# Optimization experiments

Measured on AMD Instinct MI355X. Metric: run time of the kernel, lower is better.

Reference implementation:

```python
import jax, jax.numpy as jnp
import numpy as np

CONF_THRES = 0.25
IOU_THRES = 0.45
MAX_DET = 1000
MAX_WH = 4096.0   # class offset for per-class NMS (yolov5 trick)
TOPK = 2048       # pre-NMS candidate cap (fixed-shape stand-in for max_nms)


def _xywh2xyxy(b):
    cx, cy, w, h = b[..., 0], b[..., 1], b[..., 2], b[..., 3]
    return jnp.stack([cx - w * 0.5, cy - h * 0.5, cx + w * 0.5, cy + h * 0.5], axis=-1)


def _box_iou(a, b):
    # a, b: [K, 4] in xyxy -> [K, K] pairwise IoU
    lt = jnp.maximum(a[:, None, :2], b[None, :, :2])
    rb = jnp.minimum(a[:, None, 2:], b[None, :, 2:])
    wh = jnp.clip(rb - lt, 0.0)
    inter = wh[..., 0] * wh[..., 1]
    area_a = (a[:, 2] - a[:, 0]) * (a[:, 3] - a[:, 1])
    area_b = (b[:, 2] - b[:, 0]) * (b[:, 3] - b[:, 1])
    return inter / (area_a[:, None] + area_b[None, :] - inter + 1e-7)


def _nms_single(pred):
    # pred: [N, 5+C] = (cx, cy, w, h, obj, cls...)
    obj = pred[:, 4]
    cls_prob = pred[:, 5:]
    cls_conf = jnp.max(cls_prob, axis=-1)
    cls_id = jnp.argmax(cls_prob, axis=-1)
    score = obj * cls_conf                      # conf = obj_conf * cls_conf (best class)
    valid = (obj > CONF_THRES) & (score > CONF_THRES)
    score = jnp.where(valid, score, 0.0)
    boxes = _xywh2xyxy(pred[:, :4])

    # keep top-K candidates by confidence (sorted descending)
    tops, idx = jax.lax.top_k(score, TOPK)
    boxes_k = boxes[idx]                        # [K, 4]
    cls_k = cls_id[idx]                         # [K]
    val_k = tops > 0.0

    # per-class NMS via class offset
    shifted = boxes_k + (cls_k.astype(boxes_k.dtype) * MAX_WH)[:, None]
    iou = _box_iou(shifted, shifted)            # [K, K]

    j = jnp.arange(TOPK)

    def body(i, keep):
        # if box i survives, suppress lower-scored boxes with IoU > thresh
        sup = keep[i] & (iou[i] > IOU_THRES) & (j > i)
        return keep & ~sup

    keep = jax.lax.fori_loop(0, TOPK, body, val_k)

    # gather up to MAX_DET kept detections (already score-sorted)
    fs, fi = jax.lax.top_k(jnp.where(keep, tops, -1.0), MAX_DET)
    ok = fs > 0.0
    det_boxes = jnp.where(ok[:, None], boxes_k[fi], 0.0)
    det_score = jnp.where(ok, tops[fi], 0.0)
    det_cls = jnp.where(ok, cls_k[fi].astype(det_boxes.dtype), -1.0)
    # [MAX_DET, 6] = (x1, y1, x2, y2, conf, cls); padded rows have conf 0, cls -1
    return jnp.concatenate([det_boxes, det_score[:, None], det_cls[:, None]], axis=-1)


def setup_inputs() -> dict:
    key = jax.random.key(0)
    raw = jax.random.uniform(key, (16, 25200, 85), dtype=jnp.float32)
    xy = raw[..., 0:2] * 640.0            # centers within a 640x640 image
    wh = raw[..., 2:4] * 120.0 + 2.0      # box sizes in [2, 122]
    rest = raw[..., 4:]                   # obj + class probs in [0, 1)
    pred = jnp.concatenate([xy, wh, rest], axis=-1)
    return {"pred": pred}


def reference(pred):
    return jax.vmap(_nms_single)(pred)
```

## Files before the change

kernel.cpp:

```cpp
#include <hip/hip_runtime.h>
#include <stdint.h>

#pragma clang fp contract(off)

#define BB 16
#define NN 25200
#define ROW 85
#define NCLS 80
#define TK 2048
#define SORTN 4096
#define NBIN 4096
#define MAXDET 1000
#define CONF 0.25f
#define IOUT 0.45f
#define MAXWH 4096.0f
#define SROWS 64

typedef float fvec4 __attribute__((ext_vector_type(4)));

#define AS1 __attribute__((address_space(1)))
#define AS3 __attribute__((address_space(3)))

__global__ __launch_bounds__(128) void score_kernel(const float* __restrict__ pred,
                                                    float* __restrict__ scores,
                                                    uint8_t* __restrict__ cls,
                                                    unsigned int* __restrict__ hist) {
  __shared__ __align__(16) float srow[SROWS * ROW];
  const int tile = blockIdx.x;
  const int b = blockIdx.y;
  const int tid = threadIdx.x;
  const int lane = tid & 63;
  const int row0 = tile * SROWS;
  int nrows = NN - row0;
  if (nrows > SROWS) nrows = SROWS;
  const char* gsrc = (const char*)(pred + ((size_t)b * NN + row0) * ROW);
  const int nbytes = nrows * ROW * 4;
  for (int off = tid * 16; off < nbytes; off += 128 * 16) {
    __builtin_amdgcn_global_load_lds((AS1 void*)(gsrc + off),
                                     (AS3 void*)((char*)srow + (off - lane * 16)),
                                     16, 0, 0);
  }
  __builtin_amdgcn_s_waitcnt(0);
  __syncthreads();
  if (tid < nrows) {
    const int n = row0 + tid;
    const float* r = srow + tid * ROW;
    float obj = r[4];
    float best = r[5];
    int bid = 0;
#pragma unroll
    for (int c = 1; c < NCLS; ++c) {
      float p = r[5 + c];
      if (p > best) { best = p; bid = c; }
    }
    float score = obj * best;
    bool valid = (obj > CONF) && (score > CONF);
    float sout = valid ? score : 0.0f;
    scores[(size_t)b * NN + n] = sout;
    cls[(size_t)b * NN + n] = (uint8_t)bid;
    if (valid) {
      unsigned int u = __float_as_uint(sout);
      unsigned int bin = (u - 0x3E800001u) >> 12;
      if (bin > NBIN - 1) bin = NBIN - 1;
      atomicAdd(&hist[(size_t)b * NBIN + bin], 1u);
    }
  }
}

__global__ __launch_bounds__(1024) void mega_kernel(const float* __restrict__ pred,
                                                    const float* __restrict__ scores,
                                                    const uint8_t* __restrict__ cls,
                                                    const unsigned int* __restrict__ hist,
                                                    float* __restrict__ out) {
  const int b = blockIdx.x;
  const int t = threadIdx.x;
  const int w = t >> 6;
  const int lane = t & 63;
  __shared__ unsigned long long skey[SORTN];
  __shared__ unsigned int sh[NBIN];
  __shared__ unsigned int soff[NBIN];
  __shared__ float sx1[TK], sy1[TK], sx2[TK], sy2[TK];
  __shared__ float stop[TK];
  __shared__ unsigned short scls[TK];
  __shared__ unsigned short cgrpL[TK];
  __shared__ unsigned char skp[TK];
  __shared__ int spart[1024];
  __shared__ int ccnt[NCLS];
  __shared__ int coffs[NCLS + 1];
  __shared__ int sP;

  if (t == 0) sP = 0;
  for (int i = t; i < NBIN; i += 1024) sh[i] = hist[(size_t)b * NBIN + i];
  for (int i = t; i < SORTN; i += 1024) skey[i] = 0ull;
  __syncthreads();

  int loc[4];
  int ssum = 0;
#pragma unroll
  for (int k = 0; k < 4; ++k) {
    loc[k] = (int)sh[NBIN - 1 - (4 * t + k)];
    ssum += loc[k];
  }
  spart[t] = ssum;
  __syncthreads();
  for (int o = 1; o < 1024; o <<= 1) {
    int v = (t >= o) ? spart[t - o] : 0;
    __syncthreads();
    spart[t] += v;
    __syncthreads();
  }
  int run = spart[t] - ssum;
#pragma unroll
  for (int k = 0; k < 4; ++k) {
    int bin = NBIN - 1 - (4 * t + k);
    soff[bin] = (unsigned int)run;
    if (run < TK && run + loc[k] >= TK) sP = bin;
    run += loc[k];
  }
  __syncthreads();
  const int P = sP;
  for (int i = t; i < NBIN; i += 1024) sh[i] = 0u;
  __syncthreads();

  const float* sc = scores + (size_t)b * NN;
  for (int n = t; n < NN; n += 1024) {
    unsigned int u = __float_as_uint(sc[n]);
    if (u > 0x3E800000u) {
      unsigned int bin = (u - 0x3E800001u) >> 12;
      if (bin > NBIN - 1) bin = NBIN - 1;
      if ((int)bin >= P) {
        unsigned int pos = soff[bin] + atomicAdd(&sh[bin], 1u);
        if (pos < SORTN)
          skey[pos] = ((unsigned long long)u << 32) | (unsigned int)(~n);
      }
    }
  }
  __syncthreads();

  for (int bin = P + w; bin < NBIN; bin += 16) {
    int s = (int)sh[bin];
    if (s < 2) continue;
    int base = (int)soff[bin];
    if (base >= SORTN) continue;
    if (base + s > SORTN) s = SORTN - base;
    if (s < 2) continue;
    if (s <= 64) {
      bool act = lane < s;
      unsigned long long key = act ? skey[base + lane] : 0ull;
      int rank = 0;
      for (int j = 0; j < s; ++j) {
        unsigned long long kj = skey[base + j];
        rank += (act && kj > key) ? 1 : 0;
      }
      if (act) skey[base + rank] = key;
    } else {
      for (int pass = 0; pass < s; ++pass) {
        for (int p = base + (pass & 1) + 2 * lane; p + 1 < base + s; p += 128) {
          unsigned long long a = skey[p], b2 = skey[p + 1];
          if (a < b2) { skey[p] = b2; skey[p + 1] = a; }
        }
        asm volatile("" ::: "memory");
      }
    }
    asm volatile("" ::: "memory");
  }
  __syncthreads();

  for (int i = t; i < TK; i += 1024) {
    unsigned long long key = skey[i];
    unsigned int ub = (unsigned int)(key >> 32);
    if (ub == 0u) {
      stop[i] = 0.0f;
      scls[i] = (unsigned short)0xFFFFu;
      skp[i] = 0;
      sx1[i] = 0.f; sy1[i] = 0.f; sx2[i] = 0.f; sy2[i] = 0.f;
    } else {
      int idx = (int)(~(unsigned int)key);
      stop[i] = __uint_as_float(ub);
      scls[i] = (unsigned short)cls[(size_t)b * NN + idx];
      skp[i] = 1;
      const float* rowp = pred + ((size_t)b * NN + idx) * ROW;
      float cx = rowp[0], cy = rowp[1], w2 = rowp[2], h2 = rowp[3];
      float hw = w2 * 0.5f, hh = h2 * 0.5f;
      sx1[i] = cx - hw; sy1[i] = cy - hh; sx2[i] = cx + hw; sy2[i] = cy + hh;
    }
  }
  __syncthreads();

#pragma unroll
  for (int k = 0; k < 5; ++k) {
    int c = w + 16 * k;
    int cnt = 0;
    for (int base2 = 0; base2 < TK; base2 += 64) {
      bool match = ((int)scls[base2 + lane] == c);
      cnt += (int)__popcll(__ballot(match));
    }
    if (lane == 0) ccnt[c] = cnt;
  }
  __syncthreads();
  if (t == 0) {
    int r2 = 0;
    for (int c = 0; c < NCLS; ++c) { coffs[c] = r2; r2 += ccnt[c]; }
    coffs[NCLS] = r2;
  }
  __syncthreads();
#pragma unroll
  for (int k = 0; k < 5; ++k) {
    int c = w + 16 * k;
    int run2 = coffs[c];
    for (int base2 = 0; base2 < TK; base2 += 64) {
      bool match = ((int)scls[base2 + lane] == c);
      unsigned long long bal = __ballot(match);
      int r3 = (int)__popcll(bal & ((1ull << lane) - 1ull));
      if (match) cgrpL[run2 + r3] = (unsigned short)(base2 + lane);
      run2 += (int)__popcll(bal);
    }
  }
  __syncthreads();

  for (int k = 0; k < 5; ++k) {
    int c = w + 16 * k;
    int start = coffs[c];
    int m = coffs[c + 1] - start;
    if (m <= 0) continue;
    int nq = (m + 63) >> 6;
    unsigned int km = 0;
    for (int q = 0; q < nq; ++q)
      if (lane + (q << 6) < m) km |= (1u << q);
    float b0x1 = 0.f, b0y1 = 0.f, b0x2 = 0.f, b0y2 = 0.f;
    if (lane < m) {
      int e0 = cgrpL[start + lane];
      b0x1 = sx1[e0]; b0y1 = sy1[e0]; b0x2 = sx2[e0]; b0y2 = sy2[e0];
    }
    for (int i = 0; i < m; ++i) {
      int q = i >> 6;
      unsigned int kmi = __shfl(km, i & 63);
      if (!((kmi >> q) & 1u)) continue;
      float ax1, ay1, ax2, ay2;
      if (q == 0) {
        ax1 = __shfl(b0x1, i); ay1 = __shfl(b0y1, i);
        ax2 = __shfl(b0x2, i); ay2 = __shfl(b0y2, i);
      } else {
        int ei = cgrpL[start + i];
        ax1 = sx1[ei]; ay1 = sy1[ei]; ax2 = sx2[ei]; ay2 = sy2[ei];
      }
      float aarea = (ax2 - ax1) * (ay2 - ay1);
      if ((km & 1u) && lane > i) {
        float ltx = fmaxf(ax1, b0x1), lty = fmaxf(ay1, b0y1);
        float rbx = fminf(ax2, b0x2), rby = fminf(ay2, b0y2);
        float iw = fmaxf(rbx - ltx, 0.0f);
        float ih = fmaxf(rby - lty, 0.0f);
        float inter = iw * ih;
        float barea = (b0x2 - b0x1) * (b0y2 - b0y1);
        float iou = inter / (aarea + barea - inter + 1e-7f);
        if (iou > IOUT) km &= ~1u;
      }
      for (int q2 = 1; q2 < nq; ++q2) {
        int j = lane + (q2 << 6);
        if (((km >> q2) & 1u) && j > i && j < m) {
          int ej = cgrpL[start + j];
          float jx1 = sx1[ej], jy1 = sy1[ej], jx2 = sx2[ej], jy2 = sy2[ej];
          float ltx = fmaxf(ax1, jx1), lty = fmaxf(ay1, jy1);
          float rbx = fminf(ax2, jx2), rby = fminf(ay2, jy2);
          float iw = fmaxf(rbx - ltx, 0.0f);
          float ih = fmaxf(rby - lty, 0.0f);
          float inter = iw * ih;
          float barea = (jx2 - jx1) * (jy2 - jy1);
          float iou = inter / (aarea + barea - inter + 1e-7f);
          if (iou > IOUT) km &= ~(1u << q2);
        }
      }
    }
    for (int q = 0; q < nq; ++q) {
      int j = lane + (q << 6);
      if (j < m) skp[cgrpL[start + j]] = (unsigned char)((km >> q) & 1u);
    }
  }
  __syncthreads();

  int kp0 = (int)skp[2 * t];
  int kp1 = (int)skp[2 * t + 1];
  int cnt2 = kp0 + kp1;
  spart[t] = cnt2;
  __syncthreads();
  for (int o = 1; o < 1024; o <<= 1) {
    int v = (t >= o) ? spart[t - o] : 0;
    __syncthreads();
    spart[t] += v;
    __syncthreads();
  }
  int r4 = spart[t] - cnt2;
  int K = spart[1023];
#pragma unroll
  for (int k = 0; k < 2; ++k) {
    int kp = (k == 0) ? kp0 : kp1;
    if (kp) {
      if (r4 < MAXDET) {
        int j = 2 * t + k;
        float* o = out + ((size_t)b * MAXDET + r4) * 6;
        o[0] = sx1[j]; o[1] = sy1[j]; o[2] = sx2[j]; o[3] = sy2[j];
        o[4] = stop[j];
        o[5] = (float)scls[j];
      }
      ++r4;
    }
  }
  int Kc = K < MAXDET ? K : MAXDET;
  for (int r2 = Kc + t; r2 < MAXDET; r2 += 1024) {
    float* o = out + ((size_t)b * MAXDET + r2) * 6;
    o[0] = 0.0f; o[1] = 0.0f; o[2] = 0.0f; o[3] = 0.0f; o[4] = 0.0f; o[5] = -1.0f;
  }
}

extern "C" void kernel_launch(void* const* d_in, const int* in_sizes, int n_in,
                              void* d_out, int out_size, void* d_ws, size_t ws_size,
                              hipStream_t stream) {
  const float* pred = (const float*)d_in[0];
  float* out = (float*)d_out;

  char* ws = (char*)d_ws;
  size_t off = 0;
  float*        scores = (float*)(ws + off);        off += (size_t)BB * NN * 4;
  uint8_t*      cls    = (uint8_t*)(ws + off);      off += (size_t)BB * NN;
  off = (off + 255) & ~(size_t)255;
  unsigned int* hist   = (unsigned int*)(ws + off); off += (size_t)BB * NBIN * 4;
  (void)ws_size; (void)in_sizes; (void)n_in; (void)out_size;

  hipMemsetAsync(hist, 0, (size_t)BB * NBIN * 4, stream);
  score_kernel<<<dim3((NN + SROWS - 1) / SROWS, BB), 128, 0, stream>>>(pred, scores, cls, hist);
  mega_kernel<<<BB, 1024, 0, stream>>>(pred, scores, cls, hist, out);
}
```

Measured before the change: 290.4 us.

## Split per-image mega kernel into scan, scatter, sort-emit and NMS kernels

The monolithic per-image kernel, which ran on only 16 workgroups, is split into separate kernels. A small scan kernel builds bin offsets with wave shuffles, a grid-wide scatter spreads the candidate keys across many blocks, and a multi-block sort/emit kernel ranks bins and gathers boxes into global buffers. A final kernel then runs NMS from those buffers, using a shuffle-based scan for compaction. The goal is to raise parallelism for the select/sort phase, which was serialized in 16 blocks. The cost is extra launches and round-trips through global memory, plus global-memory bubble sorts for large bins.

```diff
diff --git a/kernel.cpp b/kernel.cpp
--- a/kernel.cpp
+++ b/kernel.cpp
@@ -13,7 +13,6 @@
 #define MAXDET 1000
 #define CONF 0.25f
 #define IOUT 0.45f
-#define MAXWH 4096.0f
 #define SROWS 64
 
 typedef float fvec4 __attribute__((ext_vector_type(4)));
@@ -67,122 +66,166 @@
   }
 }
 
-__global__ __launch_bounds__(1024) void mega_kernel(const float* __restrict__ pred,
-                                                    const float* __restrict__ scores,
-                                                    const uint8_t* __restrict__ cls,
-                                                    const unsigned int* __restrict__ hist,
-                                                    float* __restrict__ out) {
+__global__ __launch_bounds__(256) void scan_kernel(const unsigned int* __restrict__ hist,
+                                                   unsigned int* __restrict__ gsoff,
+                                                   int* __restrict__ gP,
+                                                   int* __restrict__ gtot) {
+  const int b = blockIdx.x;
+  const int t = threadIdx.x;
+  const int w = t >> 6, lane = t & 63;
+  const unsigned int* h = hist + (size_t)b * NBIN;
+  unsigned int loc[16];
+  int ssum = 0;
+#pragma unroll
+  for (int k = 0; k < 16; ++k) {
+    loc[k] = h[NBIN - 1 - (16 * t + k)];
+    ssum += (int)loc[k];
+  }
+  int v = ssum;
+  for (int o = 1; o < 64; o <<= 1) { int u = __shfl_up(v, o); if (lane >= o) v += u; }
+  __shared__ int sw[4];
+  __shared__ int sfound;
+  if (t == 0) sfound = 0;
+  if (lane == 63) sw[w] = v;
+  __syncthreads();
+  int wbase = 0;
+  for (int i = 0; i < w; ++i) wbase += sw[i];
+  const int total = sw[0] + sw[1] + sw[2] + sw[3];
+  int run = wbase + v - ssum;
+#pragma unroll
+  for (int k = 0; k < 16; ++k) {
+    int bin = NBIN - 1 - (16 * t + k);
+    gsoff[(size_t)b * NBIN + bin] = (unsigned int)run;
+    int c = (int)loc[k];
+    if (run < TK && run + c >= TK) {
+      gP[b] = bin;
+      gtot[b] = run + c;
+      sfound = 1;
+    }
+    run += c;
+  }
+  __syncthreads();
+  if (t == 0 && !sfound) { gP[b] = 0; gtot[b] = total; }
+}
+
+__global__ __launch_bounds__(1024) void scatter_kernel(const float* __restrict__ scores,
+                                                       const unsigned int* __restrict__ gsoff,
+                                                       const int* __restrict__ gP,
+                                                       unsigned int* __restrict__ gcnt,
+                                                       unsigned long long* __restrict__ gskey) {
+  const int b = blockIdx.y;
+  const int n = blockIdx.x * 1024 + threadIdx.x;
+  if (n >= NN) return;
+  const unsigned int P = (unsigned int)gP[b];
+  unsigned int u = __float_as_uint(scores[(size_t)b * NN + n]);
+  if (u > 0x3E800000u) {
+    unsigned int bin = (u - 0x3E800001u) >> 12;
+    if (bin > NBIN - 1) bin = NBIN - 1;
+    if (bin >= P) {
+      unsigned int pos = gsoff[(size_t)b * NBIN + bin] +
+                         atomicAdd(&gcnt[(size_t)b * NBIN + bin], 1u);
+      if (pos < SORTN)
+        gskey[(size_t)b * SORTN + pos] = ((unsigned long long)u << 32) | (unsigned int)(~n);
+    }
+  }
+}
+
+__device__ __forceinline__ void emit_one(const float* __restrict__ pred,
+                                         const uint8_t* __restrict__ cls,
+                                         int b, int pos, unsigned long long key,
+                                         float* __restrict__ gtops,
+                                         fvec4* __restrict__ gbox,
+                                         int* __restrict__ gcls) {
+  int idx = (int)(~(unsigned int)key);
+  gtops[(size_t)b * TK + pos] = __uint_as_float((unsigned int)(key >> 32));
+  gcls[(size_t)b * TK + pos] = (int)cls[(size_t)b * NN + idx];
+  const float* rowp = pred + ((size_t)b * NN + idx) * ROW;
+  float cx = rowp[0], cy = rowp[1], w2 = rowp[2], h2 = rowp[3];
+  float hw = w2 * 0.5f, hh = h2 * 0.5f;
+  fvec4 bb4;
+  bb4[0] = cx - hw; bb4[1] = cy - hh; bb4[2] = cx + hw; bb4[3] = cy + hh;
+  gbox[(size_t)b * TK + pos] = bb4;
+}
+
+__global__ __launch_bounds__(256) void sortemit_kernel(const float* __restrict__ pred,
+                                                       const uint8_t* __restrict__ cls,
+                                                       const unsigned int* __restrict__ gsoff,
+                                                       const unsigned int* __restrict__ gcnt,
+                                                       const int* __restrict__ gP,
+                                                       unsigned long long* __restrict__ gskey,
+                                                       float* __restrict__ gtops,
+                                                       fvec4* __restrict__ gbox,
+                                                       int* __restrict__ gcls) {
+  const int b = blockIdx.y;
+  const int g = blockIdx.x;
+  const int w = threadIdx.x >> 6;
+  const int lane = threadIdx.x & 63;
+  const int P = gP[b];
+  for (int bin = P + g * 4 + w; bin < NBIN; bin += 32) {
+    int s = (int)gcnt[(size_t)b * NBIN + bin];
+    if (s <= 0) continue;
+    int base = (int)gsoff[(size_t)b * NBIN + bin];
+    if (base >= TK) continue;
+    if (base + s > SORTN) s = SORTN - base;
+    if (s <= 64) {
+      unsigned long long key = (lane < s) ? gskey[(size_t)b * SORTN + base + lane] : 0ull;
+      int rank = 0;
+      for (int jj = 0; jj < s; ++jj) {
+        unsigned long long kj = __shfl(key, jj);
+        rank += (kj > key) ? 1 : 0;
+      }
+      int pos = base + rank;
+      if (lane < s && pos < TK)
+        emit_one(pred, cls, b, pos, key, gtops, gbox, gcls);
+    } else {
+      unsigned long long* seg = gskey + (size_t)b * SORTN + base;
+      for (int pass = 0; pass < s; ++pass) {
+        for (int p = (pass & 1) + 2 * lane; p + 1 < s; p += 128) {
+          unsigned long long a = seg[p], c2 = seg[p + 1];
+          if (a < c2) { seg[p] = c2; seg[p + 1] = a; }
+        }
+        __threadfence();
+      }
+      for (int i = lane; i < s; i += 64) {
+        int pos = base + i;
+        if (pos < TK) emit_one(pred, cls, b, pos, seg[i], gtops, gbox, gcls);
+      }
+    }
+  }
+}
+
+__global__ __launch_bounds__(1024) void final_kernel(const float* __restrict__ gtops,
+                                                     const fvec4* __restrict__ gbox,
+                                                     const int* __restrict__ gcls,
+                                                     const int* __restrict__ gtot,
+                                                     float* __restrict__ out) {
   const int b = blockIdx.x;
   const int t = threadIdx.x;
   const int w = t >> 6;
   const int lane = t & 63;
-  __shared__ unsigned long long skey[SORTN];
-  __shared__ unsigned int sh[NBIN];
-  __shared__ unsigned int soff[NBIN];
   __shared__ float sx1[TK], sy1[TK], sx2[TK], sy2[TK];
   __shared__ float stop[TK];
   __shared__ unsigned short scls[TK];
   __shared__ unsigned short cgrpL[TK];
   __shared__ unsigned char skp[TK];
-  __shared__ int spart[1024];
   __shared__ int ccnt[NCLS];
   __shared__ int coffs[NCLS + 1];
-  __shared__ int sP;
-
-  if (t == 0) sP = 0;
-  for (int i = t; i < NBIN; i += 1024) sh[i] = hist[(size_t)b * NBIN + i];
-  for (int i = t; i < SORTN; i += 1024) skey[i] = 0ull;
-  __syncthreads();
-
-  int loc[4];
-  int ssum = 0;
-#pragma unroll
-  for (int k = 0; k < 4; ++k) {
-    loc[k] = (int)sh[NBIN - 1 - (4 * t + k)];
-    ssum += loc[k];
-  }
-  spart[t] = ssum;
-  __syncthreads();
-  for (int o = 1; o < 1024; o <<= 1) {
-    int v = (t >= o) ? spart[t - o] : 0;
-    __syncthreads();
-    spart[t] += v;
-    __syncthreads();
-  }
-  int run = spart[t] - ssum;
-#pragma unroll
-  for (int k = 0; k < 4; ++k) {
-    int bin = NBIN - 1 - (4 * t + k);
-    soff[bin] = (unsigned int)run;
-    if (run < TK && run + loc[k] >= TK) sP = bin;
-    run += loc[k];
-  }
-  __syncthreads();
-  const int P = sP;
-  for (int i = t; i < NBIN; i += 1024) sh[i] = 0u;
-  __syncthreads();
-
-  const float* sc = scores + (size_t)b * NN;
-  for (int n = t; n < NN; n += 1024) {
-    unsigned int u = __float_as_uint(sc[n]);
-    if (u > 0x3E800000u) {
-      unsigned int bin = (u - 0x3E800001u) >> 12;
-      if (bin > NBIN - 1) bin = NBIN - 1;
-      if ((int)bin >= P) {
-        unsigned int pos = soff[bin] + atomicAdd(&sh[bin], 1u);
-        if (pos < SORTN)
-          skey[pos] = ((unsigned long long)u << 32) | (unsigned int)(~n);
-      }
-    }
-  }
-  __syncthreads();
-
-  for (int bin = P + w; bin < NBIN; bin += 16) {
-    int s = (int)sh[bin];
-    if (s < 2) continue;
-    int base = (int)soff[bin];
-    if (base >= SORTN) continue;
-    if (base + s > SORTN) s = SORTN - base;
-    if (s < 2) continue;
-    if (s <= 64) {
-      bool act = lane < s;
-      unsigned long long key = act ? skey[base + lane] : 0ull;
-      int rank = 0;
-      for (int j = 0; j < s; ++j) {
-        unsigned long long kj = skey[base + j];
-        rank += (act && kj > key) ? 1 : 0;
-      }
-      if (act) skey[base + rank] = key;
+  __shared__ int swsum[16];
+
+  int npos = gtot[b];
+  if (npos > TK) npos = TK;
+  for (int i = t; i < TK; i += 1024) {
+    if (i < npos) {
+      fvec4 bb4 = gbox[(size_t)b * TK + i];
+      sx1[i] = bb4[0]; sy1[i] = bb4[1]; sx2[i] = bb4[2]; sy2[i] = bb4[3];
+      stop[i] = gtops[(size_t)b * TK + i];
+      scls[i] = (unsigned short)gcls[(size_t)b * TK + i];
+      skp[i] = 1;
     } else {
-      for (int pass = 0; pass < s; ++pass) {
-        for (int p = base + (pass & 1) + 2 * lane; p + 1 < base + s; p += 128) {
-          unsigned long long a = skey[p], b2 = skey[p + 1];
-          if (a < b2) { skey[p] = b2; skey[p + 1] = a; }
-        }
-        asm volatile("" ::: "memory");
-      }
-    }
-    asm volatile("" ::: "memory");
-  }
-  __syncthreads();
-
-  for (int i = t; i < TK; i += 1024) {
-    unsigned long long key = skey[i];
-    unsigned int ub = (unsigned int)(key >> 32);
-    if (ub == 0u) {
-      stop[i] = 0.0f;
+      sx1[i] = 0.f; sy1[i] = 0.f; sx2[i] = 0.f; sy2[i] = 0.f;
+      stop[i] = 0.f;
       scls[i] = (unsigned short)0xFFFFu;
       skp[i] = 0;
-      sx1[i] = 0.f; sy1[i] = 0.f; sx2[i] = 0.f; sy2[i] = 0.f;
-    } else {
-      int idx = (int)(~(unsigned int)key);
-      stop[i] = __uint_as_float(ub);
-      scls[i] = (unsigned short)cls[(size_t)b * NN + idx];
-      skp[i] = 1;
-      const float* rowp = pred + ((size_t)b * NN + idx) * ROW;
-      float cx = rowp[0], cy = rowp[1], w2 = rowp[2], h2 = rowp[3];
-      float hw = w2 * 0.5f, hh = h2 * 0.5f;
-      sx1[i] = cx - hw; sy1[i] = cy - hh; sx2[i] = cx + hw; sy2[i] = cy + hh;
     }
   }
   __syncthreads();
@@ -281,16 +324,18 @@
   int kp0 = (int)skp[2 * t];
   int kp1 = (int)skp[2 * t + 1];
   int cnt2 = kp0 + kp1;
-  spart[t] = cnt2;
-  __syncthreads();
-  for (int o = 1; o < 1024; o <<= 1) {
-    int v = (t >= o) ? spart[t - o] : 0;
-    __syncthreads();
-    spart[t] += v;
-    __syncthreads();
-  }
-  int r4 = spart[t] - cnt2;
-  int K = spart[1023];
+  int v2 = cnt2;
+  for (int o = 1; o < 64; o <<= 1) { int u2 = __shfl_up(v2, o); if (lane >= o) v2 += u2; }
+  if (lane == 63) swsum[w] = v2;
+  __syncthreads();
+  if (w == 0) {
+    int x = (lane < 16) ? swsum[lane] : 0;
+    for (int o = 1; o < 16; o <<= 1) { int u2 = __shfl_up(x, o); if (lane >= o) x += u2; }
+    if (lane < 16) swsum[lane] = x;
+  }
+  __syncthreads();
+  int r4 = (w ? swsum[w - 1] : 0) + v2 - cnt2;
+  int K = swsum[15];
 #pragma unroll
   for (int k = 0; k < 2; ++k) {
     int kp = (k == 0) ? kp0 : kp1;
@@ -320,13 +365,25 @@
 
   char* ws = (char*)d_ws;
   size_t off = 0;
-  float*        scores = (float*)(ws + off);        off += (size_t)BB * NN * 4;
-  uint8_t*      cls    = (uint8_t*)(ws + off);      off += (size_t)BB * NN;
+  float*              scores = (float*)(ws + off);              off += (size_t)BB * NN * 4;
+  uint8_t*            cls    = (uint8_t*)(ws + off);            off += (size_t)BB * NN;
   off = (off + 255) & ~(size_t)255;
-  unsigned int* hist   = (unsigned int*)(ws + off); off += (size_t)BB * NBIN * 4;
+  unsigned int*       hist   = (unsigned int*)(ws + off);       off += (size_t)BB * NBIN * 4;
+  unsigned int*       gcnt   = (unsigned int*)(ws + off);       off += (size_t)BB * NBIN * 4;
+  unsigned int*       gsoff  = (unsigned int*)(ws + off);       off += (size_t)BB * NBIN * 4;
+  unsigned long long* gskey  = (unsigned long long*)(ws + off); off += (size_t)BB * SORTN * 8;
+  float*              gtops  = (float*)(ws + off);              off += (size_t)BB * TK * 4;
+  fvec4*              gbox   = (fvec4*)(ws + off);              off += (size_t)BB * TK * 16;
+  int*                gcls   = (int*)(ws + off);                off += (size_t)BB * TK * 4;
+  int*                gP     = (int*)(ws + off);                off += (size_t)BB * 4;
+  int*                gtot   = (int*)(ws + off);                off += (size_t)BB * 4;
   (void)ws_size; (void)in_sizes; (void)n_in; (void)out_size;
 
-  hipMemsetAsync(hist, 0, (size_t)BB * NBIN * 4, stream);
+  hipMemsetAsync(hist, 0, (size_t)BB * NBIN * 4 * 2, stream);
   score_kernel<<<dim3((NN + SROWS - 1) / SROWS, BB), 128, 0, stream>>>(pred, scores, cls, hist);
-  mega_kernel<<<BB, 1024, 0, stream>>>(pred, scores, cls, hist, out);
-}
+  scan_kernel<<<BB, 256, 0, stream>>>(hist, gsoff, gP, gtot);
+  scatter_kernel<<<dim3((NN + 1023) / 1024, BB), 1024, 0, stream>>>(scores, gsoff, gP, gcnt, gskey);
+  sortemit_kernel<<<dim3(8, BB), 256, 0, stream>>>(pred, cls, gsoff, gcnt, gP, gskey,
+                                                   gtops, gbox, gcls);
+  final_kernel<<<BB, 1024, 0, stream>>>(gtops, gbox, gcls, gtot, out);
+}
```

New measurement: 289.7 us. Within noise of the previous version (-0.2%).
